# Optimization experiments

Measured on AMD Instinct MI355X. Metric: run time of the kernel, lower is better.

## Reference

```python
import jax, jax.numpy as jnp
import numpy as np

BETA = 0.95
THRESH = 1.0
SLOPE = 25.0   # fast_sigmoid surrogate slope
NUM_STEPS = 25

@jax.custom_vjp
def spike_fn(x):
    # Heaviside forward, fast_sigmoid surrogate backward
    return (x > 0).astype(x.dtype)

def _spike_fwd(x):
    return spike_fn(x), x

def _spike_bwd(x, g):
    return (g / (SLOPE * jnp.abs(x) + 1.0) ** 2,)

spike_fn.defvjp(_spike_fwd, _spike_bwd)

def lif(cur, mem):
    # snntorch Leaky, reset_mechanism='subtract': reset from previous mem, detached
    reset = jax.lax.stop_gradient((mem - THRESH > 0).astype(mem.dtype))
    mem_new = BETA * mem + cur - reset * THRESH
    spk = spike_fn(mem_new - THRESH)
    return spk, mem_new

def setup_inputs() -> dict:
    key = jax.random.key(0)
    ks = jax.random.split(key, 11)
    B, NOISE = 2048, 100
    dims = [NOISE, 128, 256, 512, 1024, 784]
    inp = {"x": jax.random.normal(ks[0], (B, NOISE), jnp.float32)}
    for i in range(5):
        bound = 1.0 / np.sqrt(dims[i]).astype(np.float32)
        inp[f"W{i+1}"] = jax.random.uniform(ks[1 + 2 * i], (dims[i + 1], dims[i]), jnp.float32, -bound, bound)
        inp[f"b{i+1}"] = jax.random.uniform(ks[2 + 2 * i], (dims[i + 1],), jnp.float32, -bound, bound)
    return inp

def reference(x, W1, b1, W2, b2, W3, b3, W4, b4, W5, b5):
    layers = [(W1, b1), (W2, b2), (W3, b3), (W4, b4), (W5, b5)]
    B = x.shape[0]
    mems0 = [jnp.zeros((B, W.shape[0]), x.dtype) for W, _ in layers]

    def step(mems, _):
        h = x
        new_mems = []
        for i, (W, b) in enumerate(layers):
            cur = jax.nn.relu(h @ W.T + b)
            spk, m = lif(cur, mems[i])
            new_mems.append(m)
            h = spk
        return new_mems, (h, jnp.tanh(new_mems[-1]))

    _, (spk_rec, mem_rec) = jax.lax.scan(step, mems0, None, length=NUM_STEPS)
    return spk_rec, mem_rec  # each [25, B, 784]
```

## Files before the change

kernel.cpp:

```cpp
#include <hip/hip_runtime.h>
#include <math.h>


typedef _Float16 f16;
typedef __attribute__((ext_vector_type(8))) short short8;
typedef __attribute__((ext_vector_type(8))) _Float16 half8;
typedef __attribute__((ext_vector_type(4))) _Float16 half4;
typedef __attribute__((ext_vector_type(4))) float f32x4;

#define B_TOTAL 2048
#define LO_SCALE 2.44140625e-4f
#define ACC_SCALE 0.015625f
#define TILE_F16 8192

__global__ __launch_bounds__(256) void gemm_relu_f32_kernel(
    const float* __restrict__ h, const float* __restrict__ W,
    const float* __restrict__ bias, float* __restrict__ out, int N, int K) {
  __shared__ float As[16][64];
  __shared__ float Bs[16][64];

  const int t = threadIdx.x;
  const int tx = t & 15;
  const int ty = t >> 4;
  const int m0 = blockIdx.y * 64;
  const int n0 = blockIdx.x * 64;
  const int lr = t >> 2;
  const int lc = (t & 3) * 4;

  float acc[4][4];
#pragma unroll
  for (int i = 0; i < 4; ++i)
#pragma unroll
    for (int j = 0; j < 4; ++j) acc[i][j] = 0.0f;

  const int ktiles = (K + 15) / 16;
  for (int kt = 0; kt < ktiles; ++kt) {
    const int kbase = kt * 16;
    {
      const float* src = h + (size_t)(m0 + lr) * K + kbase + lc;
#pragma unroll
      for (int j = 0; j < 4; ++j) {
        const int kg = kbase + lc + j;
        As[lc + j][lr] = (kg < K) ? src[j] : 0.0f;
      }
    }
    {
      const int nr = n0 + lr;
      const float* src = W + (size_t)nr * K + kbase + lc;
#pragma unroll
      for (int j = 0; j < 4; ++j) {
        const int kg = kbase + lc + j;
        Bs[lc + j][lr] = (nr < N && kg < K) ? src[j] : 0.0f;
      }
    }
    __syncthreads();
#pragma unroll
    for (int k = 0; k < 16; ++k) {
      float a[4], bb[4];
#pragma unroll
      for (int i = 0; i < 4; ++i) a[i] = As[k][ty * 4 + i];
#pragma unroll
      for (int j = 0; j < 4; ++j) bb[j] = Bs[k][tx * 4 + j];
#pragma unroll
      for (int i = 0; i < 4; ++i)
#pragma unroll
        for (int j = 0; j < 4; ++j) acc[i][j] = fmaf(a[i], bb[j], acc[i][j]);
    }
    __syncthreads();
  }

#pragma unroll
  for (int i = 0; i < 4; ++i) {
    const int m = m0 + ty * 4 + i;
#pragma unroll
    for (int j = 0; j < 4; ++j) {
      const int n = n0 + tx * 4 + j;
      if (n < N) {
        float cur = acc[i][j] + bias[n];
        out[(size_t)m * N + n] = cur > 0.0f ? cur : 0.0f;
      }
    }
  }
}

__global__ __launch_bounds__(256) void split2_kernel(
    const float* __restrict__ W, f16* __restrict__ Wc, int total, int K) {
  const int idx = blockIdx.x * 256 + threadIdx.x;
  if (idx < total) {
    const int n = idx / K;
    const int k = idx - n * K;
    const float w64 = W[idx] * 64.0f;
    const f16 hi = (f16)w64;
    const float r = w64 - (float)hi;
    const f16 lo = (f16)(r * 4096.0f);
    const size_t base = (size_t)n * 2 * K + k;
    Wc[base] = hi;
    Wc[base + K] = lo;
  }
}

__global__ __launch_bounds__(256) void lif1_kernel(
    const float* __restrict__ cur1, f16* __restrict__ s1_all) {
  const int i0 = (blockIdx.x * 256 + (int)threadIdx.x) * 4;
  const float4 c = *(const float4*)(cur1 + i0);
  const float ca[4] = {c.x, c.y, c.z, c.w};
  float m[4] = {0.0f, 0.0f, 0.0f, 0.0f};
  for (int st = 0; st < 25; ++st) {
    half4 sv;
#pragma unroll
    for (int j = 0; j < 4; ++j) {
      const float mo = m[j];
      const float reset = (mo - 1.0f > 0.0f) ? 1.0f : 0.0f;
      float mn = __fmul_rn(0.95f, mo);
      mn = __fadd_rn(mn, ca[j]);
      mn = __fsub_rn(mn, reset);
      m[j] = mn;
      sv[j] = (f16)((mn - 1.0f > 0.0f) ? 1.0f : 0.0f);
    }
    *(half4*)(s1_all + (size_t)st * (B_TOTAL * 128) + i0) = sv;
  }
}

__global__ __launch_bounds__(256) void layer_kernel(
    const f16* __restrict__ A_all,
    const f16* __restrict__ Wc,
    const float* __restrict__ bias,
    f16* __restrict__ spk_out,
    float* __restrict__ sr, float* __restrict__ mr,
    int N, int K, int mode) {
  extern __shared__ f16 Bsm[];

  const int t = threadIdx.x;
  const int lane = t & 63;
  const int w = t >> 6;
  const int wm = w >> 1;
  const int wn = w & 1;
  const int lb = blockIdx.x;
  const int m0 = (lb & 31) * 64;
  const int n0 = (lb >> 5) * 64;
  const int lrow = t >> 3;
  const int lk = (t & 7) * 8;
  const int K2 = 2 * K;
  const int nk = K >> 6;

  float bias_r[2];
#pragma unroll
  for (int j = 0; j < 2; ++j) {
    const int n = n0 + wn * 32 + j * 16 + (lane & 15);
    bias_r[j] = (n < N) ? bias[n] : 0.0f;
  }

  f32x4 acch[2][2], accl[2][2], memr[2][2];
#pragma unroll
  for (int i = 0; i < 2; ++i)
#pragma unroll
    for (int j = 0; j < 2; ++j) memr[i][j] = 0.0f;

  auto zacc = [&]() {
#pragma unroll
    for (int i = 0; i < 2; ++i)
#pragma unroll
      for (int j = 0; j < 2; ++j) {
        acch[i][j] = 0.0f;
        accl[i][j] = 0.0f;
      }
  };

  auto stage = [&](int kt, int q) {
    f16* T = Bsm + q * TILE_F16;
#pragma unroll
    for (int i = 0; i < 2; ++i) {
      const int r = lrow + 32 * i;
      const int nr = n0 + r;
      short8 vh = {}, vl = {};
      if (nr < N) {
        const f16* src = Wc + (size_t)nr * K2 + kt * 64 + lk;
        vh = *(const short8*)(src);
        vl = *(const short8*)(src + K);
      }
      const int sw = lk ^ ((r & 7) << 3);
      *(short8*)(T + r * 64 + sw) = vh;
      *(short8*)(T + (64 + r) * 64 + sw) = vl;
    }
  };

  auto compute = [&](const f16* At, int q) {
    const f16* T = Bsm + q * TILE_F16;
#pragma unroll
    for (int ks = 0; ks < 64; ks += 32) {
      const int kb = ks + (lane >> 4) * 8;
      half8 af[2], bh[2], bl[2];
#pragma unroll
      for (int i = 0; i < 2; ++i)
        af[i] = *(const half8*)(At + (size_t)i * 16 * K + ks);
#pragma unroll
      for (int j = 0; j < 2; ++j) {
        const int rr = wn * 32 + j * 16 + (lane & 15);
        const int sw = kb ^ ((rr & 7) << 3);
        bh[j] = *(const half8*)(T + rr * 64 + sw);
        bl[j] = *(const half8*)(T + (64 + rr) * 64 + sw);
      }
#pragma unroll
      for (int i = 0; i < 2; ++i)
#pragma unroll
        for (int j = 0; j < 2; ++j) {
          acch[i][j] = __builtin_amdgcn_mfma_f32_16x16x32_f16(
              af[i], bh[j], acch[i][j], 0, 0, 0);
          accl[i][j] = __builtin_amdgcn_mfma_f32_16x16x32_f16(
              af[i], bl[j], accl[i][j], 0, 0, 0);
        }
    }
  };

  auto epilogue = [&](int st) {
    const int col = lane & 15;
    const int rbase = (lane >> 4) * 4;
#pragma unroll
    for (int i = 0; i < 2; ++i) {
#pragma unroll
      for (int r = 0; r < 4; ++r) {
        const int m = m0 + wm * 32 + i * 16 + rbase + r;
#pragma unroll
        for (int j = 0; j < 2; ++j) {
          const int n = n0 + wn * 32 + j * 16 + col;
          if (n < N) {
            const float v =
                __fadd_rn(acch[i][j][r], __fmul_rn(accl[i][j][r], LO_SCALE));
            float cur = __fadd_rn(__fmul_rn(v, ACC_SCALE), bias_r[j]);
            cur = cur > 0.0f ? cur : 0.0f;
            const float mo = memr[i][j][r];
            const float reset = (mo - 1.0f > 0.0f) ? 1.0f : 0.0f;
            float mn = __fmul_rn(0.95f, mo);
            mn = __fadd_rn(mn, cur);
            mn = __fsub_rn(mn, reset);
            memr[i][j][r] = mn;
            const float s = (mn - 1.0f > 0.0f) ? 1.0f : 0.0f;
            const size_t idx = (size_t)st * (B_TOTAL * (size_t)N) +
                               (size_t)m * N + n;
            if (mode == 1) {
              sr[idx] = s;
              mr[idx] = tanhf(mn);
            } else {
              spk_out[idx] = (f16)s;
            }
          }
        }
      }
    }
  };

  const f16* Acur = A_all + (size_t)(m0 + wm * 32 + (lane & 15)) * K +
                    ((lane >> 4) * 8);
  const size_t Astep = (size_t)B_TOTAL * K;

  if (nk <= 4) {
    for (int kt = 0; kt < nk; ++kt) stage(kt, kt);
    __syncthreads();
    for (int st = 0; st < 25; ++st) {
      zacc();
      for (int kt = 0; kt < nk; ++kt) compute(Acur + kt * 64, kt);
      epilogue(st);
      Acur += Astep;
    }
  } else {
    stage(0, 0);
    __syncthreads();
    zacc();
    int kt = 0, st = 0;
    const int total = 25 * nk;
    for (int it = 0; it < total; ++it) {
      const int ktn = (kt + 1 == nk) ? 0 : kt + 1;
      const bool do_stage = (it + 1 < total);
      short8 vh[2], vl[2];
      if (do_stage) {
#pragma unroll
        for (int i = 0; i < 2; ++i) {
          const int r = lrow + 32 * i;
          const int nr = n0 + r;
          vh[i] = {};
          vl[i] = {};
          if (nr < N) {
            const f16* src = Wc + (size_t)nr * K2 + ktn * 64 + lk;
            vh[i] = *(const short8*)(src);
            vl[i] = *(const short8*)(src + K);
          }
        }
      }
      compute(Acur + kt * 64, it & 1);
      if (do_stage) {
        f16* T = Bsm + ((it + 1) & 1) * TILE_F16;
#pragma unroll
        for (int i = 0; i < 2; ++i) {
          const int r = lrow + 32 * i;
          const int sw = lk ^ ((r & 7) << 3);
          *(short8*)(T + r * 64 + sw) = vh[i];
          *(short8*)(T + (64 + r) * 64 + sw) = vl[i];
        }
      }
      __syncthreads();
      if (++kt == nk) {
        kt = 0;
        epilogue(st);
        zacc();
        ++st;
        Acur += Astep;
      }
    }
  }
}

extern "C" void kernel_launch(void* const* d_in, const int* in_sizes, int n_in,
                              void* d_out, int out_size, void* d_ws,
                              size_t ws_size, hipStream_t stream) {
  const float* x = (const float*)d_in[0];
  const float* W[5];
  const float* bi[5];
  for (int i = 0; i < 5; ++i) {
    W[i] = (const float*)d_in[1 + 2 * i];
    bi[i] = (const float*)d_in[2 + 2 * i];
  }

  const int B = B_TOTAL;
  const int Ns[5] = {128, 256, 512, 1024, 784};
  const int Ks[5] = {100, 128, 256, 512, 1024};

  char* ws = (char*)d_ws;
  size_t off = 0;
  auto alloc = [&](size_t bytes) {
    void* p = ws + off;
    off = (off + bytes + 255) & ~(size_t)255;
    return p;
  };

  float* cur1 = (float*)alloc((size_t)B * 128 * 4);
  f16* s1 = (f16*)alloc((size_t)25 * B * 128 * 2);
  f16* s2 = (f16*)alloc((size_t)25 * B * 256 * 2);
  f16* s3 = (f16*)alloc((size_t)25 * B * 512 * 2);
  f16* s4 = (f16*)alloc((size_t)25 * B * 1024 * 2);
  f16* Wc[5];
  for (int i = 1; i < 5; ++i)
    Wc[i] = (f16*)alloc((size_t)Ns[i] * Ks[i] * 2 * 2);

  float* outF = (float*)d_out;
  float* spk_rec = outF;
  float* mem_rec = outF + (size_t)25 * B * 784;

  for (int i = 1; i < 5; ++i) {
    const int total = Ns[i] * Ks[i];
    split2_kernel<<<(total + 255) / 256, 256, 0, stream>>>(W[i], Wc[i], total,
                                                           Ks[i]);
  }

  gemm_relu_f32_kernel<<<dim3(2, B / 64), 256, 0, stream>>>(x, W[0], bi[0],
                                                            cur1, 128, 100);

  lif1_kernel<<<(B * 128) / 1024, 256, 0, stream>>>(cur1, s1);

  const size_t TB = (size_t)TILE_F16 * 2;
  layer_kernel<<<32 * 4, 256, 2 * TB, stream>>>(
      s1, Wc[1], bi[1], s2, nullptr, nullptr, 256, 128, 0);
  layer_kernel<<<32 * 8, 256, 4 * TB, stream>>>(
      s2, Wc[2], bi[2], s3, nullptr, nullptr, 512, 256, 0);
  layer_kernel<<<32 * 16, 256, 2 * TB, stream>>>(
      s3, Wc[3], bi[3], s4, nullptr, nullptr, 1024, 512, 0);
  layer_kernel<<<32 * 13, 256, 2 * TB, stream>>>(
      s4, Wc[4], bi[4], nullptr, spk_rec, mem_rec, 784, 1024, 1);
}
```

Measured before the change: 1.349 ms.

## Keep full weight slab resident in LDS with templated tall-thin block tiles

The layer kernel is templated on K-tile count and N-fragment count. Each block now loads its whole weight slab (all K) into shared memory once and reuses it across all 25 timesteps. This removes the double-buffered per-iteration weight reloads and the per-tile barriers. Blocks become 128 rows by 16*NF columns with four warps split along M, which gives more blocks for the narrow final layer (784 = 49*16, so no bounds checks are needed). The cost is larger LDS per block (up to 64KB) and lower occupancy, plus the A operand is reread from global with less reuse across N.

```diff
diff --git a/kernel.cpp b/kernel.cpp
--- a/kernel.cpp
+++ b/kernel.cpp
@@ -11,7 +11,6 @@
 #define B_TOTAL 2048
 #define LO_SCALE 2.44140625e-4f
 #define ACC_SCALE 0.015625f
-#define TILE_F16 8192
 
 __global__ __launch_bounds__(256) void gemm_relu_f32_kernel(
     const float* __restrict__ h, const float* __restrict__ W,
@@ -121,6 +120,7 @@
   }
 }
 
+template <int NK, int NF>
 __global__ __launch_bounds__(256) void layer_kernel(
     const f16* __restrict__ A_all,
     const f16* __restrict__ Wc,
@@ -129,183 +129,129 @@
     float* __restrict__ sr, float* __restrict__ mr,
     int N, int K, int mode) {
   extern __shared__ f16 Bsm[];
+  constexpr int TROWS = 32 * NF;
+  constexpr int TILE = TROWS * 64;
 
   const int t = threadIdx.x;
   const int lane = t & 63;
-  const int w = t >> 6;
-  const int wm = w >> 1;
-  const int wn = w & 1;
+  const int wm = t >> 6;
   const int lb = blockIdx.x;
-  const int m0 = (lb & 31) * 64;
-  const int n0 = (lb >> 5) * 64;
+  const int m0 = (lb & 15) * 128;
+  const int n0 = (lb >> 4) * (16 * NF);
   const int lrow = t >> 3;
   const int lk = (t & 7) * 8;
   const int K2 = 2 * K;
-  const int nk = K >> 6;
-
-  float bias_r[2];
-#pragma unroll
-  for (int j = 0; j < 2; ++j) {
-    const int n = n0 + wn * 32 + j * 16 + (lane & 15);
-    bias_r[j] = (n < N) ? bias[n] : 0.0f;
-  }
-
-  f32x4 acch[2][2], accl[2][2], memr[2][2];
+
+  float bias_r[NF];
+#pragma unroll
+  for (int j = 0; j < NF; ++j) bias_r[j] = bias[n0 + j * 16 + (lane & 15)];
+
+  f32x4 acch[2][NF], accl[2][NF], memr[2][NF];
 #pragma unroll
   for (int i = 0; i < 2; ++i)
 #pragma unroll
-    for (int j = 0; j < 2; ++j) memr[i][j] = 0.0f;
-
-  auto zacc = [&]() {
-#pragma unroll
-    for (int i = 0; i < 2; ++i)
-#pragma unroll
-      for (int j = 0; j < 2; ++j) {
-        acch[i][j] = 0.0f;
-        accl[i][j] = 0.0f;
-      }
-  };
-
-  auto stage = [&](int kt, int q) {
-    f16* T = Bsm + q * TILE_F16;
-#pragma unroll
-    for (int i = 0; i < 2; ++i) {
-      const int r = lrow + 32 * i;
-      const int nr = n0 + r;
-      short8 vh = {}, vl = {};
-      if (nr < N) {
-        const f16* src = Wc + (size_t)nr * K2 + kt * 64 + lk;
-        vh = *(const short8*)(src);
-        vl = *(const short8*)(src + K);
-      }
+    for (int j = 0; j < NF; ++j) memr[i][j] = 0.0f;
+
+#pragma unroll
+  for (int kt = 0; kt < NK; ++kt) {
+    f16* T = Bsm + kt * TILE;
+    if constexpr (NF == 2) {
+      const int r = lrow;
+      const f16* src = Wc + (size_t)(n0 + r) * K2 + kt * 64 + lk;
+      const short8 vh = *(const short8*)(src);
+      const short8 vl = *(const short8*)(src + K);
       const int sw = lk ^ ((r & 7) << 3);
       *(short8*)(T + r * 64 + sw) = vh;
-      *(short8*)(T + (64 + r) * 64 + sw) = vl;
-    }
-  };
-
-  auto compute = [&](const f16* At, int q) {
-    const f16* T = Bsm + q * TILE_F16;
-#pragma unroll
-    for (int ks = 0; ks < 64; ks += 32) {
-      const int kb = ks + (lane >> 4) * 8;
-      half8 af[2], bh[2], bl[2];
-#pragma unroll
-      for (int i = 0; i < 2; ++i)
-        af[i] = *(const half8*)(At + (size_t)i * 16 * K + ks);
-#pragma unroll
-      for (int j = 0; j < 2; ++j) {
-        const int rr = wn * 32 + j * 16 + (lane & 15);
-        const int sw = kb ^ ((rr & 7) << 3);
-        bh[j] = *(const half8*)(T + rr * 64 + sw);
-        bl[j] = *(const half8*)(T + (64 + rr) * 64 + sw);
-      }
-#pragma unroll
-      for (int i = 0; i < 2; ++i)
-#pragma unroll
-        for (int j = 0; j < 2; ++j) {
-          acch[i][j] = __builtin_amdgcn_mfma_f32_16x16x32_f16(
-              af[i], bh[j], acch[i][j], 0, 0, 0);
-          accl[i][j] = __builtin_amdgcn_mfma_f32_16x16x32_f16(
-              af[i], bl[j], accl[i][j], 0, 0, 0);
-        }
-    }
-  };
-
-  auto epilogue = [&](int st) {
-    const int col = lane & 15;
-    const int rbase = (lane >> 4) * 4;
-#pragma unroll
-    for (int i = 0; i < 2; ++i) {
-#pragma unroll
-      for (int r = 0; r < 4; ++r) {
-        const int m = m0 + wm * 32 + i * 16 + rbase + r;
-#pragma unroll
-        for (int j = 0; j < 2; ++j) {
-          const int n = n0 + wn * 32 + j * 16 + col;
-          if (n < N) {
-            const float v =
-                __fadd_rn(acch[i][j][r], __fmul_rn(accl[i][j][r], LO_SCALE));
-            float cur = __fadd_rn(__fmul_rn(v, ACC_SCALE), bias_r[j]);
-            cur = cur > 0.0f ? cur : 0.0f;
-            const float mo = memr[i][j][r];
-            const float reset = (mo - 1.0f > 0.0f) ? 1.0f : 0.0f;
-            float mn = __fmul_rn(0.95f, mo);
-            mn = __fadd_rn(mn, cur);
-            mn = __fsub_rn(mn, reset);
-            memr[i][j][r] = mn;
-            const float s = (mn - 1.0f > 0.0f) ? 1.0f : 0.0f;
-            const size_t idx = (size_t)st * (B_TOTAL * (size_t)N) +
-                               (size_t)m * N + n;
-            if (mode == 1) {
-              sr[idx] = s;
-              mr[idx] = tanhf(mn);
-            } else {
-              spk_out[idx] = (f16)s;
-            }
-          }
-        }
-      }
-    }
-  };
+      *(short8*)(T + (32 + r) * 64 + sw) = vl;
+    } else {
+      const int r = lrow;
+      const int c = r & 15;
+      const f16* src =
+          Wc + (size_t)(n0 + c) * K2 + ((r < 16) ? 0 : K) + kt * 64 + lk;
+      const short8 v = *(const short8*)(src);
+      const int sw = lk ^ ((r & 7) << 3);
+      *(short8*)(T + r * 64 + sw) = v;
+    }
+  }
+  __syncthreads();
 
   const f16* Acur = A_all + (size_t)(m0 + wm * 32 + (lane & 15)) * K +
                     ((lane >> 4) * 8);
   const size_t Astep = (size_t)B_TOTAL * K;
 
-  if (nk <= 4) {
-    for (int kt = 0; kt < nk; ++kt) stage(kt, kt);
-    __syncthreads();
-    for (int st = 0; st < 25; ++st) {
-      zacc();
-      for (int kt = 0; kt < nk; ++kt) compute(Acur + kt * 64, kt);
-      epilogue(st);
-      Acur += Astep;
-    }
-  } else {
-    stage(0, 0);
-    __syncthreads();
-    zacc();
-    int kt = 0, st = 0;
-    const int total = 25 * nk;
-    for (int it = 0; it < total; ++it) {
-      const int ktn = (kt + 1 == nk) ? 0 : kt + 1;
-      const bool do_stage = (it + 1 < total);
-      short8 vh[2], vl[2];
-      if (do_stage) {
-#pragma unroll
-        for (int i = 0; i < 2; ++i) {
-          const int r = lrow + 32 * i;
-          const int nr = n0 + r;
-          vh[i] = {};
-          vl[i] = {};
-          if (nr < N) {
-            const f16* src = Wc + (size_t)nr * K2 + ktn * 64 + lk;
-            vh[i] = *(const short8*)(src);
-            vl[i] = *(const short8*)(src + K);
+  const int col = lane & 15;
+  const int rbase = (lane >> 4) * 4;
+
+  for (int st = 0; st < 25; ++st) {
+#pragma unroll
+    for (int i = 0; i < 2; ++i)
+#pragma unroll
+      for (int j = 0; j < NF; ++j) {
+        acch[i][j] = 0.0f;
+        accl[i][j] = 0.0f;
+      }
+
+#pragma unroll
+    for (int kt = 0; kt < NK; ++kt) {
+      const f16* T = Bsm + kt * TILE;
+      const f16* At = Acur + kt * 64;
+#pragma unroll
+      for (int ks = 0; ks < 64; ks += 32) {
+        const int kb = ks + (lane >> 4) * 8;
+        half8 af[2], bh[NF], bl[NF];
+#pragma unroll
+        for (int i = 0; i < 2; ++i)
+          af[i] = *(const half8*)(At + (size_t)i * 16 * K + ks);
+#pragma unroll
+        for (int j = 0; j < NF; ++j) {
+          const int rh = j * 16 + col;
+          const int rl = 16 * NF + rh;
+          bh[j] = *(const half8*)(T + rh * 64 + (kb ^ ((rh & 7) << 3)));
+          bl[j] = *(const half8*)(T + rl * 64 + (kb ^ ((rl & 7) << 3)));
+        }
+#pragma unroll
+        for (int i = 0; i < 2; ++i)
+#pragma unroll
+          for (int j = 0; j < NF; ++j) {
+            acch[i][j] = __builtin_amdgcn_mfma_f32_16x16x32_f16(
+                af[i], bh[j], acch[i][j], 0, 0, 0);
+            accl[i][j] = __builtin_amdgcn_mfma_f32_16x16x32_f16(
+                af[i], bl[j], accl[i][j], 0, 0, 0);
+          }
+      }
+    }
+
+#pragma unroll
+    for (int i = 0; i < 2; ++i) {
+#pragma unroll
+      for (int r = 0; r < 4; ++r) {
+        const int m = m0 + wm * 32 + i * 16 + rbase + r;
+#pragma unroll
+        for (int j = 0; j < NF; ++j) {
+          const int n = n0 + j * 16 + col;
+          const float v =
+              __fadd_rn(acch[i][j][r], __fmul_rn(accl[i][j][r], LO_SCALE));
+          float cur = __fadd_rn(__fmul_rn(v, ACC_SCALE), bias_r[j]);
+          cur = cur > 0.0f ? cur : 0.0f;
+          const float mo = memr[i][j][r];
+          const float reset = (mo - 1.0f > 0.0f) ? 1.0f : 0.0f;
+          float mn = __fmul_rn(0.95f, mo);
+          mn = __fadd_rn(mn, cur);
+          mn = __fsub_rn(mn, reset);
+          memr[i][j][r] = mn;
+          const float s = (mn - 1.0f > 0.0f) ? 1.0f : 0.0f;
+          const size_t idx =
+              (size_t)st * (B_TOTAL * (size_t)N) + (size_t)m * N + n;
+          if (mode == 1) {
+            sr[idx] = s;
+            mr[idx] = tanhf(mn);
+          } else {
+            spk_out[idx] = (f16)s;
           }
         }
       }
-      compute(Acur + kt * 64, it & 1);
-      if (do_stage) {
-        f16* T = Bsm + ((it + 1) & 1) * TILE_F16;
-#pragma unroll
-        for (int i = 0; i < 2; ++i) {
-          const int r = lrow + 32 * i;
-          const int sw = lk ^ ((r & 7) << 3);
-          *(short8*)(T + r * 64 + sw) = vh[i];
-          *(short8*)(T + (64 + r) * 64 + sw) = vl[i];
-        }
-      }
-      __syncthreads();
-      if (++kt == nk) {
-        kt = 0;
-        epilogue(st);
-        zacc();
-        ++st;
-        Acur += Astep;
-      }
-    }
+    }
+    Acur += Astep;
   }
 }
 
@@ -356,13 +302,12 @@
 
   lif1_kernel<<<(B * 128) / 1024, 256, 0, stream>>>(cur1, s1);
 
-  const size_t TB = (size_t)TILE_F16 * 2;
-  layer_kernel<<<32 * 4, 256, 2 * TB, stream>>>(
+  layer_kernel<2, 2><<<16 * 8, 256, 2 * 2 * 4096, stream>>>(
       s1, Wc[1], bi[1], s2, nullptr, nullptr, 256, 128, 0);
-  layer_kernel<<<32 * 8, 256, 4 * TB, stream>>>(
+  layer_kernel<4, 2><<<16 * 16, 256, 4 * 2 * 4096, stream>>>(
       s2, Wc[2], bi[2], s3, nullptr, nullptr, 512, 256, 0);
-  layer_kernel<<<32 * 16, 256, 2 * TB, stream>>>(
+  layer_kernel<8, 2><<<16 * 32, 256, 8 * 2 * 4096, stream>>>(
       s3, Wc[3], bi[3], s4, nullptr, nullptr, 1024, 512, 0);
-  layer_kernel<<<32 * 13, 256, 2 * TB, stream>>>(
+  layer_kernel<16, 1><<<16 * 49, 256, 16 * 1 * 4096, stream>>>(
       s4, Wc[4], bi[4], nullptr, spk_rec, mem_rec, 784, 1024, 1);
 }
```

Measured after the change: 2.467 ms. 82.8% more time.
